# Kernel tuning notes

Measured on AMD Instinct MI355X. Metric: run time of the kernel, lower is better.

Reference implementation:

```python
import jax, jax.numpy as jnp
import numpy as np

N = 16384      # total nodes (B graphs x 64 squares)
B = 256        # number of graphs
NODES = 64     # nodes per graph (chess board)
E = 131072     # directed edges (avg degree 8)
F_IN = 128
H = 256
GH = 4         # GAT heads
TH = 8         # transformer heads
L_GNN = 8
L_TF = 6
EPS = 1e-5


def layer_norm(x, g, b):
    m = jnp.mean(x, -1, keepdims=True)
    v = jnp.mean((x - m) ** 2, -1, keepdims=True)
    return (x - m) * jax.lax.rsqrt(v + EPS) * g + b


def setup_inputs() -> dict:
    key = jax.random.key(0)
    ks = iter(jax.random.split(key, 80))

    def nrm(shape, s=0.02):
        return jax.random.normal(next(ks), shape, jnp.float32) * s

    x = jax.random.normal(next(ks), (N, F_IN), jnp.float32)
    gid = jax.random.randint(next(ks), (E,), 0, B)
    off = jax.random.randint(next(ks), (2, E), 0, NODES)
    edge_index = gid[None, :] * NODES + off          # edges stay within a graph
    batch = jnp.arange(N, dtype=jnp.int32) // NODES
    piece_types = jax.random.randint(next(ks), (N,), 1, 7)
    return dict(
        x=x, edge_index=edge_index, batch=batch, piece_types=piece_types,
        emb_w=nrm((H, F_IN)), emb_b=nrm((H,)),
        gat_w=nrm((L_GNN, GH * H, H)), gat_as=nrm((L_GNN, GH, H)),
        gat_ad=nrm((L_GNN, GH, H)), gat_b=nrm((L_GNN, H)),
        gnn_g=jnp.ones((L_GNN, H)), gnn_beta=jnp.zeros((L_GNN, H)),
        ln1_g=jnp.ones((L_TF, H)), ln1_b=jnp.zeros((L_TF, H)),
        in_w=nrm((L_TF, 3 * H, H)), in_b=nrm((L_TF, 3 * H)),
        out_w=nrm((L_TF, H, H)), out_b=nrm((L_TF, H)),
        ln2_g=jnp.ones((L_TF, H)), ln2_b=jnp.zeros((L_TF, H)),
        ff1_w=nrm((L_TF, 4 * H, H)), ff1_b=nrm((L_TF, 4 * H)),
        ff2_w=nrm((L_TF, H, 4 * H)), ff2_b=nrm((L_TF, H)),
        pool_w=nrm((H,)), pool_b=nrm((1,)),
        vw1=nrm((H, H)), vb1=nrm((H,)), vw2=nrm((1, H)), vb2=nrm((1,)),
        pw1=nrm((H, H)), pb1=nrm((H,)), pw2=nrm((H, H)), pb2=nrm((H,)),
        uw1=nrm((H // 2, H)), ub1=nrm((H // 2,)), uw2=nrm((1, H // 2)), ub2=nrm((1,)))


def _forward(x, edge_index, batch, emb_w, emb_b, gat_w, gat_as, gat_ad, gat_b,
             gnn_g, gnn_beta, ln1_g, ln1_b, in_w, in_b, out_w, out_b, ln2_g,
             ln2_b, ff1_w, ff1_b, ff2_w, ff2_b, pool_w, pool_b, vw1, vb1, vw2,
             vb2, pw1, pb1, pw2, pb2, uw1, ub1, uw2, ub2):
    loops = jnp.arange(N, dtype=edge_index.dtype)     # GATConv add_self_loops=True
    src = jnp.concatenate([edge_index[0], loops])
    dst = jnp.concatenate([edge_index[1], loops])
    h = x @ emb_w.T + emb_b                           # [N,H] node embedding

    def gnn_layer(h, p):                              # ResidualGNNLayer
        W, a_s, a_d, bias, g, beta = p
        hp = (h @ W.T).reshape(N, GH, H)              # per-head projection
        al_s = jnp.sum(hp * a_s, -1)                  # [N,GH]
        al_d = jnp.sum(hp * a_d, -1)
        e = jax.nn.leaky_relu(al_s[src] + al_d[dst], 0.2)
        m = jax.ops.segment_max(e, dst, num_segments=N)
        ex = jnp.exp(e - m[dst])                      # segment softmax over dst
        den = jax.ops.segment_sum(ex, dst, num_segments=N)
        alpha = ex / den[dst]
        out = jax.ops.segment_sum(hp[src] * alpha[:, :, None], dst, num_segments=N)
        out = out.mean(1) + bias                      # concat=False -> head mean
        out = jax.nn.gelu(layer_norm(out, g, beta), approximate=False)
        return h + out, None                          # project = Identity

    h, _ = jax.lax.scan(gnn_layer, h, (gat_w, gat_as, gat_ad, gat_b, gnn_g, gnn_beta))

    # nn.MultiheadAttention defaults batch_first=False: axis0 (=B graphs) is the
    # sequence axis, axis1 (=64 nodes) is the batch axis — faithful to the source.
    xt = h.reshape(B, NODES, H)
    HD = H // TH

    def tf_layer(t, p):
        g1, b1, iw, ib, ow, ob, g2, b2, w1, fb1, w2, fb2 = p
        tn = layer_norm(t, g1, b1)
        q, k, v = jnp.split(tn @ iw.T + ib, 3, axis=-1)
        q = q.reshape(B, NODES, TH, HD)
        k = k.reshape(B, NODES, TH, HD)
        v = v.reshape(B, NODES, TH, HD)
        att = jnp.einsum('sbhd,tbhd->bhst', q, k) * (1.0 / HD ** 0.5)
        att = jax.nn.softmax(att, -1)
        o = jnp.einsum('bhst,tbhd->sbhd', att, v).reshape(B, NODES, H)
        t = t + (o @ ow.T + ob)
        tn = layer_norm(t, g2, b2)
        ff = jax.nn.gelu(tn @ w1.T + fb1, approximate=False) @ w2.T + fb2
        return t + ff, None

    xt, _ = jax.lax.scan(tf_layer, xt, (ln1_g, ln1_b, in_w, in_b, out_w, out_b,
                                        ln2_g, ln2_b, ff1_w, ff1_b, ff2_w, ff2_b))
    h = xt.reshape(N, H)

    # global attention pooling: softmax over ALL nodes (dim=0, as in the source)
    aw = jax.nn.softmax(h @ pool_w + pool_b[0], axis=0)
    g_rep = jax.ops.segment_sum(h * aw[:, None], batch, num_segments=B)
    value = jnp.tanh(jax.nn.gelu(g_rep @ vw1.T + vb1, approximate=False) @ vw2.T + vb2)[:, 0]
    policy = jax.nn.gelu(h @ pw1.T + pb1, approximate=False) @ pw2.T + pb2
    unc = jax.nn.softplus(jax.nn.gelu(g_rep @ uw1.T + ub1, approximate=False) @ uw2.T + ub2)[:, 0]
    return value, policy, unc


def reference(x, edge_index, batch, piece_types, emb_w, emb_b, gat_w, gat_as,
              gat_ad, gat_b, gnn_g, gnn_beta, ln1_g, ln1_b, in_w, in_b, out_w,
              out_b, ln2_g, ln2_b, ff1_w, ff1_b, ff2_w, ff2_b, pool_w, pool_b,
              vw1, vb1, vw2, vb2, pw1, pb1, pw2, pb2, uw1, ub1, uw2, ub2):
    # piece_types feeds PositionSpecificFeatureExtractor whose output is dead
    # code in the source forward (never used), so it is omitted here.
    return _forward(x, edge_index, batch, emb_w, emb_b, gat_w, gat_as, gat_ad,
                    gat_b, gnn_g, gnn_beta, ln1_g, ln1_b, in_w, in_b, out_w,
                    out_b, ln2_g, ln2_b, ff1_w, ff1_b, ff2_w, ff2_b, pool_w,
                    pool_b, vw1, vb1, vw2, vb2, pw1, pb1, pw2, pb2, uw1, ub1,
                    uw2, ub2)
```

## Files before the change

### kernel.cpp

```cpp
#include <hip/hip_runtime.h>
#include <hip/hip_bf16.h>

typedef __hip_bfloat16 bf16;
typedef __bf16 bf16x8 __attribute__((ext_vector_type(8)));
typedef float  f32x4  __attribute__((ext_vector_type(4)));

#define N_NODES 16384
#define HDIM    256
#define NE      131072
#define NE2     147456

__device__ __forceinline__ float b2f(bf16 v){ return __bfloat162float(v); }
__device__ __forceinline__ bf16  f2b(float v){ return __float2bfloat16(v); }
__device__ __forceinline__ float us2f(unsigned short u){
  union { unsigned int i; float f; } c; c.i = ((unsigned int)u) << 16; return c.f;
}
__device__ __forceinline__ unsigned short f2us(float f){
  bf16 h = __float2bfloat16(f);
  unsigned short u; __builtin_memcpy(&u, &h, 2); return u;
}
__device__ __forceinline__ float gelu_f(float x){
  return 0.5f * x * (1.0f + erff(x * 0.7071067811865476f));
}
__device__ __forceinline__ float wave_sum(float v){
  #pragma unroll
  for (int o = 32; o > 0; o >>= 1) v += __shfl_xor(v, o);
  return v;
}
__device__ __forceinline__ float wave_max(float v){
  #pragma unroll
  for (int o = 32; o > 0; o >>= 1) v = fmaxf(v, __shfl_xor(v, o));
  return v;
}

__device__ __forceinline__ float4 load4(const float* p){ return *(const float4*)p; }
__device__ __forceinline__ float4 load4(const bf16* p){
  ushort4 u = *(const ushort4*)p;
  return make_float4(us2f(u.x), us2f(u.y), us2f(u.z), us2f(u.w));
}
__device__ __forceinline__ void store4(float* p, float4 v){ *(float4*)p = v; }
__device__ __forceinline__ void store4(bf16* p, float4 v){
  ushort4 u = make_ushort4(f2us(v.x), f2us(v.y), f2us(v.z), f2us(v.w));
  *(ushort4*)p = u;
}
__device__ __forceinline__ void storev(float* p, float4 v){ *(float4*)p = v; }
__device__ __forceinline__ void storev(bf16*  p, float4 v){ store4(p, v); }

__device__ __forceinline__ void async_ld16(const bf16* g, unsigned short* l){
  __builtin_amdgcn_global_load_lds(
      (const __attribute__((address_space(1))) void*)g,
      (__attribute__((address_space(3))) void*)l, 16, 0, 0);
}

__global__ void detect_dtype(const unsigned short* __restrict__ x, int n, int* __restrict__ flags){
  int i = blockIdx.x * 256 + threadIdx.x;
  if (i < n) {
    unsigned short u = x[i];
    if ((u & 0x7F80) == 0x7F80) atomicOr(&flags[1], 1);
  }
}
struct ConvArgs {
  const void* src[35];
  unsigned short* dst[35];
  int cumg[36];
  int n[35];
};
__global__ void conv_all4(ConvArgs a, const int* __restrict__ flags){
  int gi = blockIdx.x * 256 + threadIdx.x;
  if (gi >= a.cumg[35]) return;
  int lo = 0, hi = 34;
  while (lo < hi) { int mid = (lo + hi + 1) >> 1; if (gi >= a.cumg[mid]) lo = mid; else hi = mid - 1; }
  int e0 = (gi - a.cumg[lo]) << 2;
  int n = a.n[lo];
  unsigned short* d = a.dst[lo];
  if (flags[1]) {
    const float* s = (const float*)a.src[lo];
    if (e0 + 4 <= n) {
      float4 v = *(const float4*)(s + e0);
      *(ushort4*)(d + e0) = make_ushort4(f2us(v.x), f2us(v.y), f2us(v.z), f2us(v.w));
    } else {
      for (int t = 0; t < n - e0; ++t) d[e0 + t] = f2us(s[e0 + t]);
    }
  } else {
    const unsigned short* s = (const unsigned short*)a.src[lo];
    if (e0 + 4 <= n) *(ushort4*)(d + e0) = *(const ushort4*)(s + e0);
    else for (int t = 0; t < n - e0; ++t) d[e0 + t] = s[e0 + t];
  }
}
__global__ void emit_out(const unsigned short* __restrict__ stage, void* __restrict__ out,
                         int n, const int* __restrict__ flags){
  int i = blockIdx.x * 256 + threadIdx.x;
  if (i >= n) return;
  if (flags[1]) ((float*)out)[i] = us2f(stage[i]);
  else          ((unsigned short*)out)[i] = stage[i];
}
__global__ void write_sentinel(bf16* out, float v){ out[threadIdx.x] = f2b(v); }

#define GF_GELU 1
#define GF_RES  2
#define GF_MIR  4
#define GF_ALS  8

template<typename TO, int FLAGS>
__global__ __launch_bounds__(256) void gemm2(
    const bf16* __restrict__ A, const bf16* __restrict__ W,
    const bf16* __restrict__ bias, const float* __restrict__ res,
    TO* __restrict__ C, bf16* __restrict__ C2, int M, int Nn, int K,
    const bf16* __restrict__ asp, const bf16* __restrict__ adp,
    float* __restrict__ alsp)
{
  __shared__ __align__(16) char ldsraw[36864];
  unsigned short* sA = (unsigned short*)ldsraw;
  unsigned short* sB = sA + 128 * 64;
  const int tid = threadIdx.x;
  const int wave = tid >> 6, lane = tid & 63;
  const int quad = lane >> 4, l16 = lane & 15;
  const int wm = wave & 1, wn = wave >> 1;
  const int row0 = blockIdx.y << 7, col0 = blockIdx.x << 7;
  const int lr = lane >> 3, lc = lane & 7;

  f32x4 acc[4][4] = {};

  for (int kt = 0; kt < K; kt += 64) {
    #pragma unroll
    for (int it = 0; it < 4; ++it) {
      int r0 = (wave << 5) + (it << 3);
      int rr = r0 + lr;
      int gch = lc ^ (rr & 7);
      async_ld16(A + (size_t)(row0 + rr) * K + kt + (gch << 3), sA + (r0 << 6));
      async_ld16(W + (size_t)(col0 + rr) * K + kt + (gch << 3), sB + (r0 << 6));
    }
    __syncthreads();
    #pragma unroll
    for (int kk = 0; kk < 2; ++kk) {
      bf16x8 af[4];
      #pragma unroll
      for (int i = 0; i < 4; ++i) {
        int m = (wm << 6) + (i << 4) + l16;
        af[i] = *(const bf16x8*)&sA[(m << 6) + ((((kk << 2) + quad) ^ (l16 & 7)) << 3)];
      }
      #pragma unroll
      for (int j = 0; j < 4; ++j) {
        int n = (wn << 6) + (j << 4) + l16;
        bf16x8 bfr = *(const bf16x8*)&sB[(n << 6) + ((((kk << 2) + quad) ^ (l16 & 7)) << 3)];
        #pragma unroll
        for (int i = 0; i < 4; ++i)
          acc[i][j] = __builtin_amdgcn_mfma_f32_16x16x32_bf16(af[i], bfr, acc[i][j], 0, 0, 0);
      }
    }
    __syncthreads();
  }

  float* ct = (float*)ldsraw + wave * (64 * 36);
  #pragma unroll
  for (int p = 0; p < 2; ++p) {
    #pragma unroll
    for (int i = 0; i < 4; ++i)
      #pragma unroll
      for (int r = 0; r < 4; ++r) {
        int row = (i << 4) + (quad << 2) + r;
        ct[row * 36 + l16]      = acc[i][(p << 1) + 0][r];
        ct[row * 36 + 16 + l16] = acc[i][(p << 1) + 1][r];
      }
    float4 sS = make_float4(0.f, 0.f, 0.f, 0.f);
    float4 sD = make_float4(0.f, 0.f, 0.f, 0.f);
    #pragma unroll
    for (int it2 = 0; it2 < 8; ++it2) {
      int row = (it2 << 3) + lr;
      int c4 = lc << 2;
      float4 v = *(const float4*)&ct[row * 36 + c4];
      int gcol = col0 + (wn << 6) + (p << 5) + c4;
      size_t gidx = (size_t)(row0 + (wm << 6) + row) * Nn + gcol;
      if (FLAGS & GF_ALS) {
        float asv = b2f(asp[row0 + (wm << 6) + row]);
        float adv = b2f(adp[row0 + (wm << 6) + row]);
        sS.x += asv * v.x; sS.y += asv * v.y; sS.z += asv * v.z; sS.w += asv * v.w;
        sD.x += adv * v.x; sD.y += adv * v.y; sD.z += adv * v.z; sD.w += adv * v.w;
      }
      if (bias) {
        float4 bv = load4(bias + gcol);
        v.x += bv.x; v.y += bv.y; v.z += bv.z; v.w += bv.w;
      }
      if (FLAGS & GF_GELU) {
        v.x = gelu_f(v.x); v.y = gelu_f(v.y); v.z = gelu_f(v.z); v.w = gelu_f(v.w);
      }
      if (FLAGS & GF_RES) {
        float4 rv = *(const float4*)&res[gidx];
        v.x += rv.x; v.y += rv.y; v.z += rv.z; v.w += rv.w;
      }
      storev(C + gidx, v);
      if (FLAGS & GF_MIR) store4(C2 + gidx, v);
    }
    if (FLAGS & GF_ALS) {
      #pragma unroll
      for (int o = 8; o < 64; o <<= 1) {
        sS.x += __shfl_xor(sS.x, o); sS.y += __shfl_xor(sS.y, o);
        sS.z += __shfl_xor(sS.z, o); sS.w += __shfl_xor(sS.w, o);
        sD.x += __shfl_xor(sD.x, o); sD.y += __shfl_xor(sD.y, o);
        sD.z += __shfl_xor(sD.z, o); sD.w += __shfl_xor(sD.w, o);
      }
      if (lr == 0) {
        int node = col0 + (wn << 6) + (p << 5) + (lc << 2);
        int hd2 = blockIdx.y >> 1;
        int slice = ((blockIdx.y & 1) << 1) | wm;
        *(float4*)&alsp[(size_t)((slice << 3) + hd2) * Nn + node] = sS;
        *(float4*)&alsp[(size_t)((slice << 3) + 4 + hd2) * Nn + node] = sD;
      }
    }
  }
}

__global__ void csr_count(const int* __restrict__ edst, int* __restrict__ cnt){
  int e = blockIdx.x * 256 + threadIdx.x;
  if (e < NE2) {
    int d = (e < NE) ? edst[e] : (e - NE);
    atomicAdd(&cnt[d], 1);
  }
}
__global__ __launch_bounds__(1024) void csr_scan(const int* __restrict__ cnt, int* __restrict__ off){
  __shared__ int ls[1024];
  int t = threadIdx.x;
  int base = t * 16;
  int loc[16]; int s = 0;
  #pragma unroll
  for (int j = 0; j < 16; ++j) { loc[j] = s; s += cnt[base + j]; }
  ls[t] = s;
  __syncthreads();
  for (int o = 1; o < 1024; o <<= 1) {
    int v = (t >= o) ? ls[t - o] : 0;
    __syncthreads();
    ls[t] += v;
    __syncthreads();
  }
  int pre = (t == 0) ? 0 : ls[t - 1];
  #pragma unroll
  for (int j = 0; j < 16; ++j) off[base + j] = pre + loc[j];
  if (t == 1023) off[N_NODES] = ls[1023];
}
__global__ void csr_fill(const int* __restrict__ edst, const int* __restrict__ off,
                         int* __restrict__ fillc, int* __restrict__ list){
  int e = blockIdx.x * 256 + threadIdx.x;
  if (e < NE2) {
    int d = (e < NE) ? edst[e] : (e - NE);
    int p = atomicAdd(&fillc[d], 1);
    list[off[d] + p] = e;
  }
}

#define ALF_S 68

__device__ __forceinline__ bf16x8 pack8(const float* v, float scale){
  unsigned short u[8];
  #pragma unroll
  for (int t = 0; t < 8; ++t) u[t] = f2us(v[t] * scale);
  bf16x8 r; __builtin_memcpy(&r, u, 16); return r;
}

__global__ __launch_bounds__(256) void gat_graph2(
    const int* __restrict__ esrc, const bf16* __restrict__ hpT_g,
    const int* __restrict__ off, const int* __restrict__ list,
    const float* __restrict__ alsp,
    bf16* __restrict__ msg4, int g0, int hn)
{
  __shared__ unsigned short hpT[256 * 64];
  __shared__ float alpha[64 * ALF_S];
  __shared__ float als[64], ald[64], dinv[64];

  const int hd = blockIdx.x & 3;
  const int lg = blockIdx.x >> 2;
  const int g  = g0 + lg;
  const int tid = threadIdx.x;
  const int wave = tid >> 6, lane = tid & 63;
  const int quad = lane >> 4, l16 = lane & 15;
  const int nd = tid >> 2;
  const int k4 = tid & 3;

  {
    const int rl = lane >> 3, jj = lane & 7;
    #pragma unroll
    for (int it = 0; it < 8; ++it) {
      int c = (it << 5) + (wave << 3) + rl;
      async_ld16(hpT_g + (size_t)((hd << 8) + c) * 16384 + (g << 6) + ((jj ^ (c & 7)) << 3),
                 hpT + (((it << 5) + (wave << 3)) << 6));
    }
  }
  if (tid < 128) {
    int n2 = tid & 63;
    int sd = (tid >> 6) << 2;
    float v = 0.f;
    #pragma unroll
    for (int sl = 0; sl < 4; ++sl)
      v += alsp[(size_t)((sl << 3) + sd + hd) * 16384 + (g << 6) + n2];
    if (sd) ald[n2] = v; else als[n2] = v;
  }
  #pragma unroll
  for (int idx = tid; idx < 64 * ALF_S; idx += 256) alpha[idx] = 0.f;
  __syncthreads();

  {
    int st = off[(g << 6) + nd];
    int deg = off[(g << 6) + nd + 1] - st;
    float ad = ald[nd];
    float mx = -1e30f;
    for (int e = k4; e < deg; e += 4) {
      int ed = list[st + e];
      int sl = ((ed < NE) ? esrc[ed] : (ed - NE)) - (g << 6);
      float v = als[sl] + ad;
      v = (v > 0.f) ? v : 0.2f * v;
      mx = fmaxf(mx, v);
    }
    mx = fmaxf(mx, __shfl_xor(mx, 1)); mx = fmaxf(mx, __shfl_xor(mx, 2));
    float den = 0.f;
    for (int e = k4; e < deg; e += 4) {
      int ed = list[st + e];
      int sl = ((ed < NE) ? esrc[ed] : (ed - NE)) - (g << 6);
      float v = als[sl] + ad;
      v = (v > 0.f) ? v : 0.2f * v;
      float w = __expf(v - mx);
      den += w;
      atomicAdd(&alpha[nd * ALF_S + sl], w);
    }
    den += __shfl_xor(den, 1); den += __shfl_xor(den, 2);
    if (k4 == 0) dinv[nd] = 1.0f / den;
  }
  __syncthreads();

  f32x4 acc[4][4] = {};
  #pragma unroll
  for (int kk = 0; kk < 2; ++kk) {
    bf16x8 af[4];
    #pragma unroll
    for (int i = 0; i < 4; ++i) {
      int m = (i << 4) + l16;
      const float* ap = &alpha[m * ALF_S + (kk << 5) + (quad << 3)];
      float av[8];
      float4 a0 = *(const float4*)ap, a1 = *(const float4*)(ap + 4);
      av[0]=a0.x; av[1]=a0.y; av[2]=a0.z; av[3]=a0.w;
      av[4]=a1.x; av[5]=a1.y; av[6]=a1.z; av[7]=a1.w;
      af[i] = pack8(av, dinv[m]);
    }
    #pragma unroll
    for (int j = 0; j < 4; ++j) {
      int c2 = (wave << 6) + (j << 4) + l16;
      int chunk = (kk << 2) + quad;
      bf16x8 bfr = *(const bf16x8*)&hpT[(c2 << 6) + ((chunk ^ (c2 & 7)) << 3)];
      #pragma unroll
      for (int i = 0; i < 4; ++i)
        acc[i][j] = __builtin_amdgcn_mfma_f32_16x16x32_bf16(af[i], bfr, acc[i][j], 0, 0, 0);
    }
  }

  #pragma unroll
  for (int j = 0; j < 4; ++j) {
    int col = (wave << 6) + (j << 4) + l16;
    #pragma unroll
    for (int i = 0; i < 4; ++i) {
      int rbase = (i << 4) + (quad << 2);
      #pragma unroll
      for (int r = 0; r < 4; ++r)
        msg4[((size_t)hd * hn + (lg << 6) + rbase + r) * 256 + col] = f2b(acc[i][j][r]);
    }
  }
}

__global__ __launch_bounds__(256) void gat_epi(
    const bf16* __restrict__ msg4, int hn, int n0,
    const bf16* __restrict__ bias, const bf16* __restrict__ gg, const bf16* __restrict__ gb,
    float* __restrict__ h, bf16* __restrict__ hb)
{
  int nl = blockIdx.x * 4 + (threadIdx.x >> 6);
  int lane = threadIdx.x & 63;
  int c = lane * 4;
  float4 s = make_float4(0.f, 0.f, 0.f, 0.f);
  #pragma unroll
  for (int hd = 0; hd < 4; ++hd) {
    float4 m = load4(msg4 + ((size_t)hd * hn + nl) * 256 + c);
    s.x += m.x; s.y += m.y; s.z += m.z; s.w += m.w;
  }
  float4 bv = load4(bias + c);
  float ox = s.x * 0.25f + bv.x, oy = s.y * 0.25f + bv.y;
  float oz = s.z * 0.25f + bv.z, ow = s.w * 0.25f + bv.w;
  float mean = wave_sum(ox + oy + oz + ow) * (1.0f / 256.0f);
  float dx = ox - mean, dy = oy - mean, dz = oz - mean, dw = ow - mean;
  float var = wave_sum(dx*dx + dy*dy + dz*dz + dw*dw) * (1.0f / 256.0f);
  float r = rsqrtf(var + 1e-5f);
  float4 gv = load4(gg + c); float4 b2 = load4(gb + c);
  size_t base = ((size_t)(n0 + nl)) * 256 + c;
  float4 hv = load4(h + base);
  hv.x += gelu_f(dx * r * gv.x + b2.x);
  hv.y += gelu_f(dy * r * gv.y + b2.y);
  hv.z += gelu_f(dz * r * gv.z + b2.z);
  hv.w += gelu_f(dw * r * gv.w + b2.w);
  store4(h + base, hv);
  store4(hb + base, hv);
}

__global__ __launch_bounds__(256) void ln_kernel(
    const float* __restrict__ x, bf16* __restrict__ y,
    const bf16* __restrict__ g, const bf16* __restrict__ b)
{
  int row = blockIdx.x * 4 + (threadIdx.x >> 6);
  int lane = threadIdx.x & 63;
  int c = lane * 4;
  float4 v = load4(x + (size_t)row * 256 + c);
  float mean = wave_sum(v.x + v.y + v.z + v.w) * (1.0f / 256.0f);
  float dx = v.x - mean, dy = v.y - mean, dz = v.z - mean, dw = v.w - mean;
  float var = wave_sum(dx*dx + dy*dy + dz*dz + dw*dw) * (1.0f / 256.0f);
  float r = rsqrtf(var + 1e-5f);
  float4 gv = load4(g + c); float4 bv = load4(b + c);
  store4(y + (size_t)row * 256 + c,
         make_float4(dx*r*gv.x + bv.x, dy*r*gv.y + bv.y, dz*r*gv.z + bv.z, dw*r*gv.w + bv.w));
}

#define VT_LDS 268
#define P_LDS  72

__global__ __launch_bounds__(256) void attn_mfma(
    const bf16* __restrict__ qkv, bf16* __restrict__ obuf)
{
  const int b  = blockIdx.x & 63;
  const int hh = blockIdx.x >> 6;
  __shared__ unsigned short VTs[32 * VT_LDS];
  __shared__ unsigned short Ps[4][64 * P_LDS];
  const int tid  = threadIdx.x;
  const int wave = tid >> 6, lane = tid & 63;
  const int quad = lane >> 4, l16 = lane & 15;

  {
    const bf16* vb = qkv + (size_t)(tid * 64 + b) * 768 + 512 + hh * 32;
    unsigned short vv[32];
    *(uint4*)&vv[0]  = *(const uint4*)(vb);
    *(uint4*)&vv[8]  = *(const uint4*)(vb + 8);
    *(uint4*)&vv[16] = *(const uint4*)(vb + 16);
    *(uint4*)&vv[24] = *(const uint4*)(vb + 24);
    #pragma unroll
    for (int d = 0; d < 32; ++d) VTs[d * VT_LDS + tid] = vv[d];
  }
  bf16x8 qf[4];
  #pragma unroll
  for (int i = 0; i < 4; ++i) {
    int s = (wave << 6) + (i << 4) + l16;
    qf[i] = *(const bf16x8*)(qkv + (size_t)(s * 64 + b) * 768 + hh * 32 + (quad << 3));
  }
  __syncthreads();

  const float scale = 0.17677669529663687f;
  f32x4 oacc[4][2] = {};
  float lsum[4][4] = {};
  unsigned short* Pw = &Ps[wave][0];

  for (int nt = 0; nt < 4; ++nt) {
    bf16x8 kf[4];
    #pragma unroll
    for (int j = 0; j < 4; ++j) {
      int t = (nt << 6) + (j << 4) + l16;
      kf[j] = *(const bf16x8*)(qkv + (size_t)(t * 64 + b) * 768 + 256 + hh * 32 + (quad << 3));
    }
    f32x4 zero = {0.f, 0.f, 0.f, 0.f};
    f32x4 sx[4][4];
    #pragma unroll
    for (int i = 0; i < 4; ++i)
      #pragma unroll
      for (int j = 0; j < 4; ++j)
        sx[i][j] = __builtin_amdgcn_mfma_f32_16x16x32_bf16(qf[i], kf[j], zero, 0, 0, 0);
    #pragma unroll
    for (int i = 0; i < 4; ++i) {
      #pragma unroll
      for (int r = 0; r < 4; ++r) {
        float p[4]; float rs = 0.f;
        #pragma unroll
        for (int j = 0; j < 4; ++j) {
          float sc = fminf(fmaxf(sx[i][j][r] * scale, -60.f), 60.f);
          p[j] = __expf(sc);
          rs += p[j];
        }
        #pragma unroll
        for (int o = 1; o < 16; o <<= 1) rs += __shfl_xor(rs, o);
        lsum[i][r] += rs;
        int row = (i << 4) + (quad << 2) + r;
        #pragma unroll
        for (int j = 0; j < 4; ++j)
          Pw[row * P_LDS + (j << 4) + l16] = f2us(p[j]);
      }
    }
    #pragma unroll
    for (int kk = 0; kk < 2; ++kk) {
      bf16x8 vf[2];
      #pragma unroll
      for (int j2 = 0; j2 < 2; ++j2)
        vf[j2] = *(const bf16x8*)&VTs[((j2 << 4) + l16) * VT_LDS + (nt << 6) + (kk << 5) + (quad << 3)];
      #pragma unroll
      for (int i2 = 0; i2 < 4; ++i2) {
        bf16x8 pf = *(const bf16x8*)&Pw[((i2 << 4) + l16) * P_LDS + (kk << 5) + (quad << 3)];
        #pragma unroll
        for (int j2 = 0; j2 < 2; ++j2)
          oacc[i2][j2] = __builtin_amdgcn_mfma_f32_16x16x32_bf16(pf, vf[j2], oacc[i2][j2], 0, 0, 0);
      }
    }
  }
  #pragma unroll
  for (int i = 0; i < 4; ++i) {
    #pragma unroll
    for (int r = 0; r < 4; ++r) {
      int srow = (wave << 6) + (i << 4) + (quad << 2) + r;
      float inv = 1.0f / lsum[i][r];
      #pragma unroll
      for (int j2 = 0; j2 < 2; ++j2)
        obuf[(size_t)(srow * 64 + b) * 256 + hh * 32 + (j2 << 4) + l16] = f2b(oacc[i][j2][r] * inv);
    }
  }
}

__global__ __launch_bounds__(256) void pool_logit(
    const float* __restrict__ h, const bf16* __restrict__ pw, const bf16* __restrict__ pb,
    float* __restrict__ logits)
{
  int n = blockIdx.x * 4 + (threadIdx.x >> 6); int lane = threadIdx.x & 63;
  float4 hv = load4(h + (size_t)n * 256 + lane * 4);
  float4 wv = load4(pw + lane * 4);
  float acc = wave_sum(hv.x*wv.x + hv.y*wv.y + hv.z*wv.z + hv.w*wv.w);
  if (lane == 0) logits[n] = acc + b2f(pb[0]);
}
__global__ __launch_bounds__(1024) void pool_reduce(
    const float* __restrict__ logits, float* __restrict__ red)
{
  __shared__ float sm[16];
  int t = threadIdx.x;
  float m = -1e30f;
  for (int i = t; i < N_NODES; i += 1024) m = fmaxf(m, logits[i]);
  m = wave_max(m);
  if ((t & 63) == 0) sm[t >> 6] = m;
  __syncthreads();
  if (t == 0) { float mm = sm[0]; for (int i = 1; i < 16; ++i) mm = fmaxf(mm, sm[i]); sm[0] = mm; }
  __syncthreads();
  float gmax = sm[0];
  __syncthreads();
  float s = 0.f;
  for (int i = t; i < N_NODES; i += 1024) s += expf(logits[i] - gmax);
  s = wave_sum(s);
  if ((t & 63) == 0) sm[t >> 6] = s;
  __syncthreads();
  if (t == 0) { float ss = 0.f; for (int i = 0; i < 16; ++i) ss += sm[i]; red[0] = gmax; red[1] = 1.0f / ss; }
}
__global__ __launch_bounds__(256) void pool_grep(
    const float* __restrict__ h, const float* __restrict__ logits,
    const float* __restrict__ red, bf16* __restrict__ g_rep)
{
  __shared__ float w[64];
  int g = blockIdx.x; int tid = threadIdx.x;
  if (tid < 64) w[tid] = expf(logits[g * 64 + tid] - red[0]) * red[1];
  __syncthreads();
  float acc = 0.f;
  for (int nd = 0; nd < 64; ++nd) acc += h[((size_t)g * 64 + nd) * 256 + tid] * w[nd];
  g_rep[(size_t)g * 256 + tid] = f2b(acc);
}
__global__ __launch_bounds__(256) void head_value(
    const float* __restrict__ vt, const bf16* __restrict__ w2, const bf16* __restrict__ b2,
    bf16* __restrict__ out)
{
  int gidx = blockIdx.x * 4 + (threadIdx.x >> 6); int lane = threadIdx.x & 63;
  float acc = 0.f;
  #pragma unroll
  for (int j = 0; j < 4; ++j) { int c = j * 64 + lane; acc += vt[(size_t)gidx * 256 + c] * b2f(w2[c]); }
  acc = wave_sum(acc);
  if (lane == 0) out[gidx] = f2b(tanhf(acc + b2f(b2[0])));
}
__global__ __launch_bounds__(256) void head_unc(
    const float* __restrict__ ut, const bf16* __restrict__ w2, const bf16* __restrict__ b2,
    bf16* __restrict__ out)
{
  int gidx = blockIdx.x * 4 + (threadIdx.x >> 6); int lane = threadIdx.x & 63;
  float acc = 0.f;
  #pragma unroll
  for (int j = 0; j < 2; ++j) { int c = j * 64 + lane; acc += ut[(size_t)gidx * 128 + c] * b2f(w2[c]); }
  acc = wave_sum(acc);
  if (lane == 0) {
    float x = acc + b2f(b2[0]);
    float sp = (x > 20.f) ? x : log1pf(expf(x));
    out[gidx] = f2b(sp);
  }
}

extern "C" void kernel_launch(void* const* d_in, const int* in_sizes, int n_in,
                              void* d_out, int out_size, void* d_ws, size_t ws_size,
                              hipStream_t stream)
{
  (void)out_size;
  const int* eidx = (const int*)d_in[1];

  char* ws = (char*)d_ws;
  size_t wo = 0;
  auto alloc = [&](size_t bytes) -> char* {
    char* p = ws + wo; wo += (bytes + 255) & ~(size_t)255; return p;
  };
  int*   flags = (int*)alloc(256);
  int*   cnt   = (int*)alloc((size_t)N_NODES * 4);
  int*   fillc = (int*)alloc((size_t)N_NODES * 4);
  size_t zero_end = wo;

  bf16* conv[38] = {};
  static const int fidx[35] = {0,4,5,6,7,8,9,10,11,12,13,14,15,16,17,18,19,
                               20,21,22,23,24,25,26,27,28,29,30,31,32,33,34,35,36,37};
  for (int j = 0; j < 35; ++j) {
    int idx = fidx[j];
    conv[idx] = (bf16*)alloc((size_t)in_sizes[idx] * 2);
  }
  float* h     = (float*)alloc((size_t)N_NODES * 256 * 4);
  bf16*  hb    = (bf16*) alloc((size_t)N_NODES * 256 * 2);
  bf16*  big   = (bf16*) alloc((size_t)N_NODES * 1024 * 2);
  const int OUT_ELEMS = 256 + N_NODES * 256 + 256;
  bf16*  tn     = (bf16*)alloc((size_t)N_NODES * 256 * 2);
  bf16*  ostage = (bf16*)alloc((size_t)OUT_ELEMS * 2);
  int*   off   = (int*)alloc((size_t)(N_NODES + 1) * 4);
  int*   list  = (int*)alloc((size_t)NE2 * 4);
  float* logits= (float*)alloc((size_t)N_NODES * 4);
  float* redb  = (float*)alloc(256);
  bf16*  g_rep = (bf16*)alloc((size_t)256 * 256 * 2);
  float* val_t = (float*)alloc((size_t)256 * 256 * 4);
  float* unc_t = (float*)alloc((size_t)256 * 128 * 4);
  float* alsp  = (float*)alloc((size_t)32 * N_NODES * 4);
  size_t base_needed = wo;

  if (n_in != 38)                   { write_sentinel<<<1,256,0,stream>>>((bf16*)d_out, 4.f);  return; }
  if (in_sizes[0] != N_NODES * 128) { write_sentinel<<<1,256,0,stream>>>((bf16*)d_out, 8.f);  return; }
  if (in_sizes[1] != 2 * NE)        { write_sentinel<<<1,256,0,stream>>>((bf16*)d_out, 16.f); return; }
  if (ws_size < base_needed)        { write_sentinel<<<1,256,0,stream>>>((bf16*)d_out, 32.f); return; }

  size_t msg_bytes = (size_t)4 * N_NODES * 256 * 2;
  bf16* msg4; int halves;
  if (ws_size >= base_needed + msg_bytes + 256) {
    msg4 = (bf16*)alloc(msg_bytes); halves = 1;
  } else {
    msg4 = tn; halves = 2;
  }

  hipMemsetAsync(d_ws, 0, zero_end, stream);

  detect_dtype<<<256, 256, 0, stream>>>((const unsigned short*)d_in[0], 65536, flags);
  {
    ConvArgs ca;
    int cum = 0;
    for (int j = 0; j < 35; ++j) {
      int idx = fidx[j];
      ca.src[j] = d_in[idx];
      ca.dst[j] = (unsigned short*)conv[idx];
      ca.cumg[j] = cum;
      ca.n[j] = in_sizes[idx];
      cum += (in_sizes[idx] + 3) >> 2;
    }
    ca.cumg[35] = cum;
    conv_all4<<<(cum + 255) / 256, 256, 0, stream>>>(ca, flags);
  }
  const bf16 *xb = conv[0], *emb_w = conv[4], *emb_b = conv[5], *gat_w = conv[6],
             *gat_as = conv[7], *gat_ad = conv[8], *gat_b = conv[9], *gnn_g = conv[10],
             *gnn_beta = conv[11], *ln1_g = conv[12], *ln1_b = conv[13], *in_w = conv[14],
             *in_b = conv[15], *out_w = conv[16], *out_b = conv[17], *ln2_g = conv[18],
             *ln2_b = conv[19], *ff1_w = conv[20], *ff1_b = conv[21], *ff2_w = conv[22],
             *ff2_b = conv[23], *pool_w = conv[24], *pool_b = conv[25],
             *vw1 = conv[26], *vb1 = conv[27], *vw2 = conv[28], *vb2 = conv[29],
             *pw1 = conv[30], *pb1 = conv[31], *pw2 = conv[32], *pb2 = conv[33],
             *uw1 = conv[34], *ub1 = conv[35], *uw2 = conv[36], *ub2 = conv[37];

  bf16* qkv  = big;
  bf16* obuf = big + (size_t)N_NODES * 768;
  bf16* hpT_g = big;
  bf16* ffb  = big;
  bf16* o_val = ostage;
  bf16* o_pol = ostage + 256;
  bf16* o_unc = ostage + 256 + (size_t)N_NODES * 256;

  csr_count<<<(NE2 + 255) / 256, 256, 0, stream>>>(eidx + NE, cnt);
  csr_scan<<<1, 1024, 0, stream>>>(cnt, off);
  csr_fill<<<(NE2 + 255) / 256, 256, 0, stream>>>(eidx + NE, off, fillc, list);

  gemm2<float, GF_MIR><<<dim3(2, 128), 256, 0, stream>>>(
      xb, emb_w, emb_b, nullptr, h, hb, N_NODES, 256, 128,
      nullptr, nullptr, nullptr);

  const int gph = 256 / halves;
  const int hn  = N_NODES / halves;
  for (int l = 0; l < 8; ++l) {
    gemm2<bf16, GF_ALS><<<dim3(128, 8), 256, 0, stream>>>(
        gat_w + (size_t)l * 1024 * 256, hb, nullptr, nullptr, hpT_g, nullptr,
        1024, N_NODES, 256, gat_as + l * 1024, gat_ad + l * 1024, alsp);
    for (int ph = 0; ph < halves; ++ph) {
      gat_graph2<<<gph * 4, 256, 0, stream>>>(eidx, hpT_g, off, list, alsp,
          msg4, ph * gph, hn);
      gat_epi<<<hn / 4, 256, 0, stream>>>(msg4, hn, ph * hn,
          gat_b + l * 256, gnn_g + l * 256, gnn_beta + l * 256, h, hb);
    }
  }

  for (int l = 0; l < 6; ++l) {
    ln_kernel<<<N_NODES / 4, 256, 0, stream>>>(h, tn, ln1_g + l * 256, ln1_b + l * 256);
    gemm2<bf16, 0><<<dim3(6, 128), 256, 0, stream>>>(
        tn, in_w + (size_t)l * 768 * 256, in_b + l * 768, nullptr, qkv, nullptr, N_NODES, 768, 256,
        nullptr, nullptr, nullptr);
    attn_mfma<<<512, 256, 0, stream>>>(qkv, obuf);
    gemm2<float, GF_RES><<<dim3(2, 128), 256, 0, stream>>>(
        obuf, out_w + (size_t)l * 256 * 256, out_b + l * 256, h, h, nullptr, N_NODES, 256, 256,
        nullptr, nullptr, nullptr);
    ln_kernel<<<N_NODES / 4, 256, 0, stream>>>(h, tn, ln2_g + l * 256, ln2_b + l * 256);
    gemm2<bf16, GF_GELU><<<dim3(8, 128), 256, 0, stream>>>(
        tn, ff1_w + (size_t)l * 1024 * 256, ff1_b + l * 1024, nullptr, ffb, nullptr, N_NODES, 1024, 256,
        nullptr, nullptr, nullptr);
    if (l < 5)
      gemm2<float, GF_RES><<<dim3(2, 128), 256, 0, stream>>>(
          ffb, ff2_w + (size_t)l * 256 * 1024, ff2_b + l * 256, h, h, nullptr, N_NODES, 256, 1024,
          nullptr, nullptr, nullptr);
    else
      gemm2<float, GF_RES | GF_MIR><<<dim3(2, 128), 256, 0, stream>>>(
          ffb, ff2_w + (size_t)l * 256 * 1024, ff2_b + l * 256, h, h, hb, N_NODES, 256, 1024,
          nullptr, nullptr, nullptr);
  }

  pool_logit<<<N_NODES / 4, 256, 0, stream>>>(h, pool_w, pool_b, logits);
  pool_reduce<<<1, 1024, 0, stream>>>(logits, redb);
  pool_grep<<<256, 256, 0, stream>>>(h, logits, redb, g_rep);
  gemm2<float, GF_GELU><<<dim3(2, 2), 256, 0, stream>>>(
      g_rep, vw1, vb1, nullptr, val_t, nullptr, 256, 256, 256,
      nullptr, nullptr, nullptr);
  head_value<<<64, 256, 0, stream>>>(val_t, vw2, vb2, o_val);
  gemm2<float, GF_GELU><<<dim3(1, 2), 256, 0, stream>>>(
      g_rep, uw1, ub1, nullptr, unc_t, nullptr, 256, 128, 256,
      nullptr, nullptr, nullptr);
  head_unc<<<64, 256, 0, stream>>>(unc_t, uw2, ub2, o_unc);
  gemm2<bf16, GF_GELU><<<dim3(2, 128), 256, 0, stream>>>(
      hb, pw1, pb1, nullptr, tn, nullptr, N_NODES, 256, 256,
      nullptr, nullptr, nullptr);
  gemm2<bf16, 0><<<dim3(2, 128), 256, 0, stream>>>(
      tn, pw2, pb2, nullptr, o_pol, nullptr, N_NODES, 256, 256,
      nullptr, nullptr, nullptr);

  emit_out<<<(OUT_ELEMS + 255) / 256, 256, 0, stream>>>(
      (const unsigned short*)ostage, d_out, OUT_ELEMS, flags);
}
```

Measured before the change: 1.582 ms.

## Fuse residual GEMMs with following LayerNorm via full-row-tile GEMM kernel

Adds a GEMM kernel where each block computes a full 64x256 output tile. Its epilogue adds bias and residual, writes h, and computes the next LayerNorm into tn. It replaces the out-proj and FF2 residual GEMMs plus the separate ln_kernel launches, and the first LN1 is folded into the last GAT epilogue. This removes an extra read of h and the launches per layer. The cost is only 256 blocks, no double-buffering, and large LDS use per block, which may reduce occupancy compared with the 2x128 grid.

```diff
diff --git a/kernel.cpp b/kernel.cpp
--- a/kernel.cpp
+++ b/kernel.cpp
@@ -210,6 +210,111 @@
   }
 }
 
+__global__ __launch_bounds__(256) void gemm_rln(
+    const bf16* __restrict__ A, const bf16* __restrict__ W,
+    const bf16* __restrict__ bias, float* __restrict__ h,
+    bf16* __restrict__ tn, const bf16* __restrict__ lng,
+    const bf16* __restrict__ lnb, int K)
+{
+  __shared__ __align__(16) char ldsraw[66560];
+  unsigned short* sA = (unsigned short*)ldsraw;
+  unsigned short* sB = sA + 64 * 64;
+  const int tid = threadIdx.x;
+  const int wave = tid >> 6, lane = tid & 63;
+  const int quad = lane >> 4, l16 = lane & 15;
+  const int row0 = blockIdx.x << 6;
+  const int lr = lane >> 3, lc = lane & 7;
+
+  f32x4 acc[4][4] = {};
+
+  for (int kt = 0; kt < K; kt += 64) {
+    #pragma unroll
+    for (int it = 0; it < 2; ++it) {
+      int r0 = (wave << 4) + (it << 3);
+      int rr = r0 + lr;
+      int gch = lc ^ (rr & 7);
+      async_ld16(A + (size_t)(row0 + rr) * K + kt + (gch << 3), sA + (r0 << 6));
+    }
+    #pragma unroll
+    for (int it = 0; it < 8; ++it) {
+      int r0 = (wave << 6) + (it << 3);
+      int rr = r0 + lr;
+      int gch = lc ^ (rr & 7);
+      async_ld16(W + (size_t)rr * K + kt + (gch << 3), sB + (r0 << 6));
+    }
+    __syncthreads();
+    #pragma unroll
+    for (int kk = 0; kk < 2; ++kk) {
+      bf16x8 af[4];
+      #pragma unroll
+      for (int i = 0; i < 4; ++i) {
+        int m = (i << 4) + l16;
+        af[i] = *(const bf16x8*)&sA[(m << 6) + ((((kk << 2) + quad) ^ (l16 & 7)) << 3)];
+      }
+      #pragma unroll
+      for (int j = 0; j < 4; ++j) {
+        int n = (wave << 6) + (j << 4) + l16;
+        bf16x8 bfr = *(const bf16x8*)&sB[(n << 6) + ((((kk << 2) + quad) ^ (l16 & 7)) << 3)];
+        #pragma unroll
+        for (int i = 0; i < 4; ++i)
+          acc[i][j] = __builtin_amdgcn_mfma_f32_16x16x32_bf16(af[i], bfr, acc[i][j], 0, 0, 0);
+      }
+    }
+    __syncthreads();
+  }
+
+  float* ct = (float*)ldsraw;
+  #pragma unroll
+  for (int j = 0; j < 4; ++j) {
+    int col = (wave << 6) + (j << 4) + l16;
+    #pragma unroll
+    for (int i = 0; i < 4; ++i)
+      #pragma unroll
+      for (int r = 0; r < 4; ++r)
+        ct[((i << 4) + (quad << 2) + r) * 260 + col] = acc[i][j][r];
+  }
+  __syncthreads();
+
+  const int row = tid >> 2, q = tid & 3;
+  const int c0 = q << 6;
+  size_t gr = (size_t)(row0 + row) * 256 + c0;
+  float4 v[16];
+  float s1 = 0.f;
+  #pragma unroll
+  for (int k = 0; k < 16; ++k) {
+    float4 cv = *(const float4*)&ct[row * 260 + c0 + (k << 2)];
+    float4 bv = load4(bias + c0 + (k << 2));
+    float4 rv = *(const float4*)&h[gr + (k << 2)];
+    v[k].x = cv.x + bv.x + rv.x;
+    v[k].y = cv.y + bv.y + rv.y;
+    v[k].z = cv.z + bv.z + rv.z;
+    v[k].w = cv.w + bv.w + rv.w;
+    *(float4*)&h[gr + (k << 2)] = v[k];
+    s1 += v[k].x + v[k].y + v[k].z + v[k].w;
+  }
+  s1 += __shfl_xor(s1, 1); s1 += __shfl_xor(s1, 2);
+  float mean = s1 * (1.0f / 256.0f);
+  float s2 = 0.f;
+  #pragma unroll
+  for (int k = 0; k < 16; ++k) {
+    float dx = v[k].x - mean, dy = v[k].y - mean, dz = v[k].z - mean, dw = v[k].w - mean;
+    s2 += dx * dx + dy * dy + dz * dz + dw * dw;
+  }
+  s2 += __shfl_xor(s2, 1); s2 += __shfl_xor(s2, 2);
+  float rstd = rsqrtf(s2 * (1.0f / 256.0f) + 1e-5f);
+  #pragma unroll
+  for (int k = 0; k < 16; ++k) {
+    float4 gv = load4(lng + c0 + (k << 2));
+    float4 bv2 = load4(lnb + c0 + (k << 2));
+    float4 y;
+    y.x = (v[k].x - mean) * rstd * gv.x + bv2.x;
+    y.y = (v[k].y - mean) * rstd * gv.y + bv2.y;
+    y.z = (v[k].z - mean) * rstd * gv.z + bv2.z;
+    y.w = (v[k].w - mean) * rstd * gv.w + bv2.w;
+    store4(tn + gr + (k << 2), y);
+  }
+}
+
 __global__ void csr_count(const int* __restrict__ edst, int* __restrict__ cnt){
   int e = blockIdx.x * 256 + threadIdx.x;
   if (e < NE2) {
@@ -366,7 +471,8 @@
 __global__ __launch_bounds__(256) void gat_epi(
     const bf16* __restrict__ msg4, int hn, int n0,
     const bf16* __restrict__ bias, const bf16* __restrict__ gg, const bf16* __restrict__ gb,
-    float* __restrict__ h, bf16* __restrict__ hb)
+    float* __restrict__ h, bf16* __restrict__ hb,
+    const bf16* __restrict__ lng, const bf16* __restrict__ lnb, bf16* __restrict__ tno)
 {
   int nl = blockIdx.x * 4 + (threadIdx.x >> 6);
   int lane = threadIdx.x & 63;
@@ -393,6 +499,15 @@
   hv.w += gelu_f(dw * r * gv.w + b2.w);
   store4(h + base, hv);
   store4(hb + base, hv);
+  if (lng) {
+    float m2 = wave_sum(hv.x + hv.y + hv.z + hv.w) * (1.0f / 256.0f);
+    float ex = hv.x - m2, ey = hv.y - m2, ez = hv.z - m2, ew = hv.w - m2;
+    float v2 = wave_sum(ex*ex + ey*ey + ez*ez + ew*ew) * (1.0f / 256.0f);
+    float r2 = rsqrtf(v2 + 1e-5f);
+    float4 g2 = load4(lng + c); float4 bb = load4(lnb + c);
+    store4(tno + base, make_float4(ex*r2*g2.x + bb.x, ey*r2*g2.y + bb.y,
+                                   ez*r2*g2.z + bb.z, ew*r2*g2.w + bb.w));
+  }
 }
 
 __global__ __launch_bounds__(256) void ln_kernel(
@@ -683,31 +798,34 @@
     gemm2<bf16, GF_ALS><<<dim3(128, 8), 256, 0, stream>>>(
         gat_w + (size_t)l * 1024 * 256, hb, nullptr, nullptr, hpT_g, nullptr,
         1024, N_NODES, 256, gat_as + l * 1024, gat_ad + l * 1024, alsp);
+    const bf16* lng = (l == 7 && halves == 1) ? ln1_g : nullptr;
+    const bf16* lnb = (l == 7 && halves == 1) ? ln1_b : nullptr;
     for (int ph = 0; ph < halves; ++ph) {
       gat_graph2<<<gph * 4, 256, 0, stream>>>(eidx, hpT_g, off, list, alsp,
           msg4, ph * gph, hn);
       gat_epi<<<hn / 4, 256, 0, stream>>>(msg4, hn, ph * hn,
-          gat_b + l * 256, gnn_g + l * 256, gnn_beta + l * 256, h, hb);
-    }
-  }
+          gat_b + l * 256, gnn_g + l * 256, gnn_beta + l * 256, h, hb,
+          lng, lnb, tn);
+    }
+  }
+  if (halves == 2)
+    ln_kernel<<<N_NODES / 4, 256, 0, stream>>>(h, tn, ln1_g, ln1_b);
 
   for (int l = 0; l < 6; ++l) {
-    ln_kernel<<<N_NODES / 4, 256, 0, stream>>>(h, tn, ln1_g + l * 256, ln1_b + l * 256);
     gemm2<bf16, 0><<<dim3(6, 128), 256, 0, stream>>>(
         tn, in_w + (size_t)l * 768 * 256, in_b + l * 768, nullptr, qkv, nullptr, N_NODES, 768, 256,
         nullptr, nullptr, nullptr);
     attn_mfma<<<512, 256, 0, stream>>>(qkv, obuf);
-    gemm2<float, GF_RES><<<dim3(2, 128), 256, 0, stream>>>(
-        obuf, out_w + (size_t)l * 256 * 256, out_b + l * 256, h, h, nullptr, N_NODES, 256, 256,
-        nullptr, nullptr, nullptr);
-    ln_kernel<<<N_NODES / 4, 256, 0, stream>>>(h, tn, ln2_g + l * 256, ln2_b + l * 256);
+    gemm_rln<<<N_NODES / 64, 256, 0, stream>>>(
+        obuf, out_w + (size_t)l * 256 * 256, out_b + l * 256, h, tn,
+        ln2_g + l * 256, ln2_b + l * 256, 256);
     gemm2<bf16, GF_GELU><<<dim3(8, 128), 256, 0, stream>>>(
         tn, ff1_w + (size_t)l * 1024 * 256, ff1_b + l * 1024, nullptr, ffb, nullptr, N_NODES, 1024, 256,
         nullptr, nullptr, nullptr);
     if (l < 5)
-      gemm2<float, GF_RES><<<dim3(2, 128), 256, 0, stream>>>(
-          ffb, ff2_w + (size_t)l * 256 * 1024, ff2_b + l * 256, h, h, nullptr, N_NODES, 256, 1024,
-          nullptr, nullptr, nullptr);
+      gemm_rln<<<N_NODES / 64, 256, 0, stream>>>(
+          ffb, ff2_w + (size_t)l * 256 * 1024, ff2_b + l * 256, h, tn,
+          ln1_g + (l + 1) * 256, ln1_b + (l + 1) * 256, 1024);
     else
       gemm2<float, GF_RES | GF_MIR><<<dim3(2, 128), 256, 0, stream>>>(
           ffb, ff2_w + (size_t)l * 256 * 1024, ff2_b + l * 256, h, h, hb, N_NODES, 256, 1024,
```

Result: faster. 1.550 ms (-2.0%).
